# Performance work log

Measured on AMD Instinct MI355X. Metric: run time of the kernel, lower is better.

Reference implementation:

```python
import jax, jax.numpy as jnp
import numpy as np

B, H, W, C = 32, 56, 56, 384
NH, WS, SS = 12, 7, 3
DH = C // NH
N = WS * WS
HID = 4 * C
SCALE = DH ** -0.5


def _make_attn_mask(h, w, ws, ss):
    img = np.zeros((h, w), dtype=np.float32)
    cnt = 0
    for hs in (slice(0, -ws), slice(-ws, -ss), slice(-ss, None)):
        for wsl in (slice(0, -ws), slice(-ws, -ss), slice(-ss, None)):
            img[hs, wsl] = cnt
            cnt += 1
    mw = img.reshape(h // ws, ws, w // ws, ws).transpose(0, 2, 1, 3).reshape(-1, ws * ws)
    diff = mw[:, None, :] - mw[:, :, None]  # (nW, n, n)
    return np.where(diff != 0, np.float32(-100.0), np.float32(0.0))


def _make_rel_pos_index(ws):
    coords = np.stack(np.meshgrid(np.arange(ws), np.arange(ws), indexing='ij')).reshape(2, -1)
    rel = (coords[:, :, None] - coords[:, None, :]).transpose(1, 2, 0)  # (n, n, 2)
    rel[..., 0] += ws - 1
    rel[..., 1] += ws - 1
    rel[..., 0] *= 2 * ws - 1
    return rel.sum(-1)  # (n, n)


ATTN_MASK = jnp.asarray(_make_attn_mask(H, W, WS, SS))          # (nW, n, n)
REL_IDX = jnp.asarray(_make_rel_pos_index(WS))                   # (n, n)


def layernorm(x, g, b, eps):
    mu = jnp.mean(x, axis=-1, keepdims=True)
    var = jnp.var(x, axis=-1, keepdims=True)
    return (x - mu) * jax.lax.rsqrt(var + eps) * g + b


def window_partition(x, ws):
    b, h, w, c = x.shape
    x = x.reshape(b, h // ws, ws, w // ws, ws, c)
    return x.transpose(0, 1, 3, 2, 4, 5).reshape(-1, ws, ws, c)


def window_reverse(windows, ws, h, w):
    b = windows.shape[0] // ((h // ws) * (w // ws))
    x = windows.reshape(b, h // ws, w // ws, ws, ws, -1)
    return x.transpose(0, 1, 3, 2, 4, 5).reshape(b, h, w, -1)


def setup_inputs() -> dict:
    key = jax.random.key(0)
    ks = jax.random.split(key, 8)
    d = {
        'x': jax.random.normal(ks[0], (B, H * W, C), dtype=jnp.float32),
        'ln1_g': jnp.ones((C,), jnp.float32), 'ln1_b': jnp.zeros((C,), jnp.float32),
        'qkv_w': jax.random.normal(ks[1], (C, 3 * C), jnp.float32) * 0.02,
        'qkv_b': jnp.zeros((3 * C,), jnp.float32),
        'proj_w': jax.random.normal(ks[2], (C, C), jnp.float32) * 0.02,
        'proj_b': jnp.zeros((C,), jnp.float32),
        'rpb_table': jax.random.normal(ks[3], ((2 * WS - 1) ** 2, NH), jnp.float32) * 0.02,
        'ln2_g': jnp.ones((C,), jnp.float32), 'ln2_b': jnp.zeros((C,), jnp.float32),
        'ffln_g': jnp.ones((C,), jnp.float32), 'ffln_b': jnp.zeros((C,), jnp.float32),
        'ff1_w': jax.random.normal(ks[4], (C, HID), jnp.float32) * 0.02,
        'ff1_b': jnp.zeros((HID,), jnp.float32),
        'ff2_w': jax.random.normal(ks[5], (HID, C), jnp.float32) * 0.02,
        'ff2_b': jnp.zeros((C,), jnp.float32),
    }
    return d


def reference(x, ln1_g, ln1_b, qkv_w, qkv_b, proj_w, proj_b, rpb_table,
              ln2_g, ln2_b, ffln_g, ffln_b, ff1_w, ff1_b, ff2_w, ff2_b):
    b = x.shape[0]
    shortcut = x
    xn = layernorm(x, ln1_g, ln1_b, 1e-5).reshape(b, H, W, C)
    shifted = jnp.roll(xn, shift=(-SS, -SS), axis=(1, 2))
    xw = window_partition(shifted, WS).reshape(-1, N, C)  # (b*nW, n, c)
    Bw = xw.shape[0]
    nW = Bw // b

    qkv = (xw @ qkv_w + qkv_b).reshape(Bw, N, 3, NH, DH).transpose(2, 0, 3, 1, 4)
    q, k, v = qkv[0], qkv[1], qkv[2]  # (Bw, nh, n, dh)
    dots = jnp.einsum('bhnd,bhmd->bhnm', q, k) * SCALE

    bias = rpb_table[REL_IDX.reshape(-1)].reshape(N, N, NH).transpose(2, 0, 1)  # (nh, n, n)
    attn = dots + bias[None]
    attn = attn.reshape(b, nW, NH, N, N) + ATTN_MASK[None, :, None, :, :]
    attn = jax.nn.softmax(attn.reshape(Bw, NH, N, N), axis=-1)

    out = jnp.einsum('bhnm,bhmd->bhnd', attn, v)
    out = out.transpose(0, 2, 1, 3).reshape(Bw, N, C)
    out = out @ proj_w + proj_b

    out = window_reverse(out.reshape(-1, WS, WS, C), WS, H, W)
    out = jnp.roll(out, shift=(SS, SS), axis=(1, 2)).reshape(b, H * W, C)

    x = shortcut + out
    y = layernorm(x, ln2_g, ln2_b, 1e-5)
    y = layernorm(y, ffln_g, ffln_b, 1e-6)
    y = jax.nn.gelu(y @ ff1_w + ff1_b, approximate=False) @ ff2_w + ff2_b
    return x + y
```

## Files before the change

### kernel.cpp

```cpp
#include <hip/hip_runtime.h>
#include <hip/hip_bf16.h>

typedef short bf16x8 __attribute__((ext_vector_type(8)));
typedef short short4v __attribute__((ext_vector_type(4)));
typedef float f32x4  __attribute__((ext_vector_type(4)));

static constexpr float SCALE = 0.17677669529663687f;

__device__ __forceinline__ void gload_lds16(const void* g, void* l) {
  __builtin_amdgcn_global_load_lds(
      (const __attribute__((address_space(1))) unsigned int*)g,
      (__attribute__((address_space(3))) unsigned int*)l, 16, 0, 0);
}

__device__ __forceinline__ size_t win_to_nat(int t) {
  int win = t / 49; int n = t - win * 49;
  int bb = win >> 6; int wimg = win & 63;
  int hb = wimg >> 3, wb = wimg & 7;
  int nr = n / 7, nc = n - nr * 7;
  int hh = hb * 7 + nr + 3; if (hh >= 56) hh -= 56;
  int ww = wb * 7 + nc + 3; if (ww >= 56) ww -= 56;
  return (size_t)bb * 3136 + (size_t)hh * 56 + ww;
}

__device__ __forceinline__ float gelu_fast(float x) {
  float t = __expf(-1.702f * x);
  return x / (1.f + t);
}

__global__ __launch_bounds__(256)
void k_transpose(const float* __restrict__ W, __hip_bfloat16* __restrict__ Wt,
                 int K, int N) {
  __shared__ float tile[32][33];
  int tx = threadIdx.x & 31, ty = threadIdx.x >> 5;
  int tc = blockIdx.x, tr = blockIdx.y;
#pragma unroll
  for (int r = 0; r < 32; r += 8)
    tile[r + ty][tx] = W[(size_t)(tr * 32 + r + ty) * N + tc * 32 + tx];
  __syncthreads();
#pragma unroll
  for (int r = 0; r < 32; r += 8)
    Wt[(size_t)(tc * 32 + r + ty) * K + tr * 32 + tx] =
        __float2bfloat16(tile[tx][r + ty]);
}

__global__ __launch_bounds__(256)
void k_ln1(const float* __restrict__ x, const float* __restrict__ gw,
           const float* __restrict__ bw, __hip_bfloat16* __restrict__ xw) {
  int lane = threadIdx.x & 63;
  int t = blockIdx.x * 4 + (threadIdx.x >> 6);
  size_t nt = win_to_nat(t);
  const float* xr = x + nt * 384;
  float4 a  = *(const float4*)(xr + lane * 4);
  float2 c2 = *(const float2*)(xr + 256 + lane * 2);
  float v[6] = {a.x, a.y, a.z, a.w, c2.x, c2.y};
  int c0 = lane * 4, c1 = 256 + lane * 2;
  int ch[6] = {c0, c0 + 1, c0 + 2, c0 + 3, c1, c1 + 1};
  float s = 0.f, q = 0.f;
#pragma unroll
  for (int i = 0; i < 6; i++) { s += v[i]; q += v[i] * v[i]; }
#pragma unroll
  for (int m = 1; m < 64; m <<= 1) { s += __shfl_xor(s, m); q += __shfl_xor(q, m); }
  float mean = s * (1.f / 384.f);
  float rstd = rsqrtf(q * (1.f / 384.f) - mean * mean + 1e-5f);
  __hip_bfloat16* o = xw + (size_t)t * 384;
#pragma unroll
  for (int i = 0; i < 6; i++)
    o[ch[i]] = __float2bfloat16((v[i] - mean) * rstd * gw[ch[i]] + bw[ch[i]]);
}

__global__ __launch_bounds__(256)
void k_ln2ff(const float* __restrict__ xres, const float* __restrict__ g2,
             const float* __restrict__ b2, const float* __restrict__ gf,
             const float* __restrict__ bf_, __hip_bfloat16* __restrict__ yln) {
  int lane = threadIdx.x & 63;
  int t = blockIdx.x * 4 + (threadIdx.x >> 6);
  const float* xr = xres + (size_t)t * 384;
  float4 a  = *(const float4*)(xr + lane * 4);
  float2 c2 = *(const float2*)(xr + 256 + lane * 2);
  float v[6] = {a.x, a.y, a.z, a.w, c2.x, c2.y};
  int c0 = lane * 4, c1 = 256 + lane * 2;
  int ch[6] = {c0, c0 + 1, c0 + 2, c0 + 3, c1, c1 + 1};
  float s = 0.f, q = 0.f;
#pragma unroll
  for (int i = 0; i < 6; i++) { s += v[i]; q += v[i] * v[i]; }
#pragma unroll
  for (int m = 1; m < 64; m <<= 1) { s += __shfl_xor(s, m); q += __shfl_xor(q, m); }
  float mean = s * (1.f / 384.f);
  float rstd = rsqrtf(q * (1.f / 384.f) - mean * mean + 1e-5f);
  float y1[6];
  s = 0.f; q = 0.f;
#pragma unroll
  for (int i = 0; i < 6; i++) {
    y1[i] = (v[i] - mean) * rstd * g2[ch[i]] + b2[ch[i]];
    s += y1[i]; q += y1[i] * y1[i];
  }
#pragma unroll
  for (int m = 1; m < 64; m <<= 1) { s += __shfl_xor(s, m); q += __shfl_xor(q, m); }
  float m2 = s * (1.f / 384.f);
  float r2 = rsqrtf(q * (1.f / 384.f) - m2 * m2 + 1e-6f);
  __hip_bfloat16* o = yln + (size_t)t * 384;
#pragma unroll
  for (int i = 0; i < 6; i++)
    o[ch[i]] = __float2bfloat16((y1[i] - m2) * r2 * gf[ch[i]] + bf_[ch[i]]);
}

enum { EPI_QKV = 0, EPI_PROJ = 1, EPI_FF1 = 2, EPI_FF2 = 3 };

template <int EPI>
__global__ __launch_bounds__(256)
void k_gemm(const __hip_bfloat16* __restrict__ A, const __hip_bfloat16* __restrict__ Wt,
            const float* __restrict__ bias, int K, int nCol, int cpx,
            const float* __restrict__ aux,
            float* __restrict__ out_f,
            __hip_bfloat16* __restrict__ out_b) {
  __shared__ __hip_bfloat16 LB[24576];
  int tid = threadIdx.x;
  int lane = tid & 63, w = tid >> 6;
  int g = lane >> 4, r16 = lane & 15;
  int wr = w >> 1, wc = w & 1;

  int bid = blockIdx.x;
  int wg = (bid & 7) * cpx + (bid >> 3);
  int rB = wg / nCol;
  int rowBlk = rB * 128;
  int colBlk = (wg - rB * nCol) * 128;

  int s2 = (tid & 7) ^ ((tid >> 3) & 7);
  int srow = 2 * (tid >> 3) + (s2 >> 2);
  int cch = s2 & 3;
  const __hip_bfloat16* PA = A + (size_t)(rowBlk + srow) * K + cch * 8;
  const __hip_bfloat16* PB = Wt + (size_t)(colBlk + srow) * K + cch * 8;

#define STG(NB, T)                                                            \
  {                                                                           \
    int k0s = (T) << 5;                                                       \
    _Pragma("unroll") for (int j = 0; j < 2; j++) {                           \
      gload_lds16(PA + (size_t)j * 64 * K + k0s, &LB[(NB) * 4096 + j * 2048 + w * 512]); \
      gload_lds16(PB + (size_t)j * 64 * K + k0s, &LB[12288 + (NB) * 4096 + j * 2048 + w * 512]); \
    }                                                                         \
  }

  int rslot = (g + ((r16 & 1) << 2)) ^ (r16 >> 1);
  int aBase = (wr * 32 + (r16 >> 1)) * 64 + rslot * 8;
  int bBase = 12288 + (wc * 32 + (r16 >> 1)) * 64 + rslot * 8;

  f32x4 acc[4][4] = {};
  const int nt = K >> 5;

  STG(0, 0)
  STG(1, 1)

#define STEP(CB, SB, T)                                                       \
  {                                                                           \
    if ((T) + 1 < nt) {                                                       \
      asm volatile("s_waitcnt vmcnt(4)" ::: "memory");                        \
    } else {                                                                  \
      asm volatile("s_waitcnt vmcnt(0)" ::: "memory");                        \
    }                                                                         \
    __builtin_amdgcn_s_barrier();                \
    asm volatile("" ::: "memory");                                            \
    bf16x8 a[4], b[4];                                                        \
    _Pragma("unroll") for (int mi = 0; mi < 4; mi++)                          \
      a[mi] = *(const bf16x8*)(&LB[(CB) * 4096 + aBase + mi * 512]);          \
    _Pragma("unroll") for (int ni = 0; ni < 4; ni++)                          \
      b[ni] = *(const bf16x8*)(&LB[(CB) * 4096 + bBase + ni * 512]);          \
    if ((T) + 2 < nt) STG(SB, (T) + 2)                                        \
    __builtin_amdgcn_s_setprio(1);                                            \
    _Pragma("unroll") for (int mi = 0; mi < 4; mi++)                          \
      _Pragma("unroll") for (int ni = 0; ni < 4; ni++)                        \
        acc[mi][ni] = __builtin_amdgcn_mfma_f32_16x16x32_bf16(                \
            b[ni], a[mi], acc[mi][ni], 0, 0, 0);                              \
    __builtin_amdgcn_s_setprio(0);                                            \
  }

  for (int t = 0; t < nt; t += 3) {
    STEP(0, 2, t)
    STEP(1, 0, t + 1)
    STEP(2, 1, t + 2)
  }
#undef STEP
#undef STG

  if constexpr (EPI == EPI_QKV || EPI == EPI_FF1) {
    __hip_bfloat16* EP = &LB[w * 4096];
#pragma unroll
    for (int ni = 0; ni < 4; ni++) {
      float4 b4 = *(const float4*)(bias + colBlk + wc * 64 + ni * 16 + g * 4);
#pragma unroll
      for (int mi = 0; mi < 4; mi++) {
        float v0 = acc[mi][ni][0] + b4.x, v1 = acc[mi][ni][1] + b4.y,
              v2 = acc[mi][ni][2] + b4.z, v3 = acc[mi][ni][3] + b4.w;
        if constexpr (EPI == EPI_FF1) {
          v0 = gelu_fast(v0); v1 = gelu_fast(v1);
          v2 = gelu_fast(v2); v3 = gelu_fast(v3);
        }
        short4v s4 = {(short)__bfloat16_as_ushort(__float2bfloat16(v0)),
                      (short)__bfloat16_as_ushort(__float2bfloat16(v1)),
                      (short)__bfloat16_as_ushort(__float2bfloat16(v2)),
                      (short)__bfloat16_as_ushort(__float2bfloat16(v3))};
        int row = mi * 16 + r16;
        int ch8 = (ni * 2 + (g >> 1)) ^ (row & 7);
        *(short4v*)(&EP[row * 64 + ch8 * 8 + (g & 1) * 4]) = s4;
      }
    }
#pragma unroll
    for (int j = 0; j < 8; j++) {
      int r = j * 8 + (lane >> 3);
      bf16x8 vv = *(const bf16x8*)(&EP[r * 64 + ((lane & 7) ^ (r & 7)) * 8]);
      int grow = rowBlk + wr * 64 + r;
      int col0 = colBlk + wc * 64 + (lane & 7) * 8;
      if constexpr (EPI == EPI_QKV) {
        int winr = grow / 49, nn = grow - winr * 49;
        int which = col0 / 384; int rem = col0 - which * 384;
        int hh = rem >> 5, dd = rem & 31;
        size_t off = (((size_t)winr * 12 + hh) * 49 + nn) * 32 + dd;
        *(bf16x8*)(out_b + (size_t)which * 38535168u + off) = vv;
      } else {
        *(bf16x8*)(out_b + (size_t)grow * 1536 + col0) = vv;
      }
    }
  } else {
    float* EPF = (float*)LB + w * 2048;
#pragma unroll
    for (int half = 0; half < 2; half++) {
#pragma unroll
      for (int ni = 0; ni < 4; ni++) {
        float4 b4 = *(const float4*)(bias + colBlk + wc * 64 + ni * 16 + g * 4);
#pragma unroll
        for (int mi2 = 0; mi2 < 2; mi2++) {
          int mi = half * 2 + mi2;
          f32x4 v = acc[mi][ni];
          v[0] += b4.x; v[1] += b4.y; v[2] += b4.z; v[3] += b4.w;
          int row = mi2 * 16 + r16;
          int ch4 = (ni * 4 + g) ^ r16;
          *(f32x4*)(&EPF[row * 64 + ch4 * 4]) = v;
        }
      }
#pragma unroll
      for (int j = 0; j < 8; j++) {
        int r = j * 4 + g;
        f32x4 vv = *(const f32x4*)(&EPF[r * 64 + ((r16 ^ (r & 15)) * 4)]);
        int grow = rowBlk + wr * 64 + half * 32 + r;
        int col0 = colBlk + wc * 64 + r16 * 4;
        if constexpr (EPI == EPI_PROJ) {
          size_t nt2 = win_to_nat(grow);
          const float4 a4 = *(const float4*)(aux + nt2 * 384 + col0);
          float4 o4 = {vv[0] + a4.x, vv[1] + a4.y, vv[2] + a4.z, vv[3] + a4.w};
          *(float4*)(out_f + nt2 * 384 + col0) = o4;
        } else {
          const float4 a4 = *(const float4*)(aux + (size_t)grow * 384 + col0);
          float4 o4 = {vv[0] + a4.x, vv[1] + a4.y, vv[2] + a4.z, vv[3] + a4.w};
          *(float4*)(out_f + (size_t)grow * 384 + col0) = o4;
        }
      }
    }
  }
}

__global__ __launch_bounds__(256)
void k_attn(const __hip_bfloat16* __restrict__ q, const __hip_bfloat16* __restrict__ k,
            const __hip_bfloat16* __restrict__ v, const float* __restrict__ rpb,
            __hip_bfloat16* __restrict__ o) {
  __shared__ __hip_bfloat16 P[4][64][72];
  int tid = threadIdx.x;
  int lane = tid & 63, wave = tid >> 6;
  int g = lane >> 4, r16 = lane & 15;
  int gid = blockIdx.x * 4 + wave;
  int wi = gid / 12, h = gid - (gid / 12) * 12;
  int wimg = wi & 63;
  int hb = wimg >> 3, wb = wimg & 7;
  size_t base = ((size_t)wi * 12 + h) * (49 * 32);
  const __hip_bfloat16* qb = q + base;
  const __hip_bfloat16* kb = k + base;
  const __hip_bfloat16* vb = v + base;

  bf16x8 zf = {0, 0, 0, 0, 0, 0, 0, 0};
  bf16x8 qf[4], kf[4];
#pragma unroll
  for (int mi = 0; mi < 4; mi++) {
    int row = mi * 16 + r16;
    qf[mi] = (row < 49) ? *(const bf16x8*)(qb + row * 32 + g * 8) : zf;
    kf[mi] = (row < 49) ? *(const bf16x8*)(kb + row * 32 + g * 8) : zf;
  }
  f32x4 fz = {0.f, 0.f, 0.f, 0.f};
  f32x4 S[4][4];
#pragma unroll
  for (int mi = 0; mi < 4; mi++)
#pragma unroll
    for (int ni = 0; ni < 4; ni++)
      S[mi][ni] = __builtin_amdgcn_mfma_f32_16x16x32_bf16(qf[mi], kf[ni], fz, 0, 0, 0);

  int kiA[4], kjA[4], rkA[4], cvA[4];
#pragma unroll
  for (int ni = 0; ni < 4; ni++) {
    int col = ni * 16 + r16;
    cvA[ni] = (col < 49);
    int ki = col / 7, kj = col - (col / 7) * 7;
    kiA[ni] = ki; kjA[ni] = kj;
    int hg = hb * 7 + ki, wg = wb * 7 + kj;
    int rh = (hg < 49) ? 0 : ((hg < 53) ? 1 : 2);
    int rw = (wg < 49) ? 0 : ((wg < 53) ? 1 : 2);
    rkA[ni] = rh * 3 + rw;
  }

#pragma unroll
  for (int mi = 0; mi < 4; mi++) {
#pragma unroll
    for (int rr = 0; rr < 4; rr++) {
      int row = mi * 16 + g * 4 + rr;
      float sv[4];
      float mx = -1e30f;
      int qi = row / 7, qj = row - (row / 7) * 7;
      int hgq = hb * 7 + qi, wgq = wb * 7 + qj;
      int rhq = (hgq < 49) ? 0 : ((hgq < 53) ? 1 : 2);
      int rwq = (wgq < 49) ? 0 : ((wgq < 53) ? 1 : 2);
      int rq = rhq * 3 + rwq;
#pragma unroll
      for (int ni = 0; ni < 4; ni++) {
        float s = -1e30f;
        if (row < 49 && cvA[ni]) {
          int idx = (qi - kiA[ni] + 6) * 13 + (qj - kjA[ni] + 6);
          float maskv = (rq != rkA[ni]) ? -100.f : 0.f;
          s = S[mi][ni][rr] * SCALE + rpb[idx * 12 + h] + maskv;
        }
        sv[ni] = s;
        mx = fmaxf(mx, s);
      }
#pragma unroll
      for (int m = 1; m <= 8; m <<= 1) mx = fmaxf(mx, __shfl_xor(mx, m));
      float sum = 0.f;
#pragma unroll
      for (int ni = 0; ni < 4; ni++) {
        float p = __expf(sv[ni] - mx);
        sv[ni] = p; sum += p;
      }
#pragma unroll
      for (int m = 1; m <= 8; m <<= 1) sum += __shfl_xor(sum, m);
      float inv = 1.f / sum;
#pragma unroll
      for (int ni = 0; ni < 4; ni++)
        P[wave][row][ni * 16 + r16] = __float2bfloat16(sv[ni] * inv);
    }
  }

  f32x4 O[4][2] = {};
#pragma unroll
  for (int ks = 0; ks < 2; ks++) {
    bf16x8 pf[4];
#pragma unroll
    for (int mi = 0; mi < 4; mi++)
      pf[mi] = *(const bf16x8*)(&P[wave][mi * 16 + r16][ks * 32 + g * 8]);
#pragma unroll
    for (int ni = 0; ni < 2; ni++) {
      bf16x8 vf = zf;
#pragma unroll
      for (int j = 0; j < 8; j++) {
        int m = ks * 32 + g * 8 + j;
        if (m < 49) vf[j] = ((const short*)vb)[m * 32 + ni * 16 + r16];
      }
#pragma unroll
      for (int mi = 0; mi < 4; mi++)
        O[mi][ni] = __builtin_amdgcn_mfma_f32_16x16x32_bf16(pf[mi], vf, O[mi][ni], 0, 0, 0);
    }
  }

#pragma unroll
  for (int mi = 0; mi < 4; mi++)
#pragma unroll
    for (int rr = 0; rr < 4; rr++) {
      int row = mi * 16 + g * 4 + rr;
      if (row < 49) {
#pragma unroll
        for (int ni = 0; ni < 2; ni++) {
          int col = ni * 16 + r16;
          o[(((size_t)wi * 49 + row) * 12 + h) * 32 + col] = __float2bfloat16(O[mi][ni][rr]);
        }
      }
    }
}

extern "C" void kernel_launch(void* const* d_in, const int* in_sizes, int n_in,
                              void* d_out, int out_size, void* d_ws, size_t ws_size,
                              hipStream_t stream) {
  const float* x      = (const float*)d_in[0];
  const float* ln1_g  = (const float*)d_in[1];
  const float* ln1_b  = (const float*)d_in[2];
  const float* qkv_w  = (const float*)d_in[3];
  const float* qkv_b  = (const float*)d_in[4];
  const float* proj_w = (const float*)d_in[5];
  const float* proj_b = (const float*)d_in[6];
  const float* rpb    = (const float*)d_in[7];
  const float* ln2_g  = (const float*)d_in[8];
  const float* ln2_b  = (const float*)d_in[9];
  const float* ffg    = (const float*)d_in[10];
  const float* ffb    = (const float*)d_in[11];
  const float* ff1_w  = (const float*)d_in[12];
  const float* ff1_b  = (const float*)d_in[13];
  const float* ff2_w  = (const float*)d_in[14];
  const float* ff2_b  = (const float*)d_in[15];
  float* out = (float*)d_out;

  char* ws = (char*)d_ws;
  __hip_bfloat16* xw     = (__hip_bfloat16*)ws;
  __hip_bfloat16* qbuf   = (__hip_bfloat16*)(ws + 77070336u);
  __hip_bfloat16* kbuf   = qbuf + 38535168u;
  __hip_bfloat16* vbuf   = kbuf + 38535168u;
  __hip_bfloat16* attn_o = xw;
  __hip_bfloat16* hbuf   = (__hip_bfloat16*)ws;
  float*          x_res  = (float*)(ws + 308281344u);
  __hip_bfloat16* yln    = (__hip_bfloat16*)(ws + 462422016u);
  __hip_bfloat16* qkv_wt = (__hip_bfloat16*)(ws + 539492352u);
  __hip_bfloat16* proj_wt = qkv_wt + 442368u;
  __hip_bfloat16* ff1_wt  = proj_wt + 147456u;
  __hip_bfloat16* ff2_wt  = ff1_wt + 589824u;

  k_transpose<<<dim3(1152 / 32, 384 / 32), dim3(256), 0, stream>>>(qkv_w, qkv_wt, 384, 1152);
  k_transpose<<<dim3(384 / 32, 384 / 32), dim3(256), 0, stream>>>(proj_w, proj_wt, 384, 384);
  k_transpose<<<dim3(1536 / 32, 384 / 32), dim3(256), 0, stream>>>(ff1_w, ff1_wt, 384, 1536);
  k_transpose<<<dim3(384 / 32, 1536 / 32), dim3(256), 0, stream>>>(ff2_w, ff2_wt, 1536, 384);

  k_ln1<<<dim3(25088), dim3(256), 0, stream>>>(x, ln1_g, ln1_b, xw);

  k_gemm<EPI_QKV><<<dim3(7056), dim3(256), 0, stream>>>(xw, qkv_wt, qkv_b, 384, 9, 7056 / 8,
                                                        nullptr, nullptr, qbuf);
  k_attn<<<dim3(6144), dim3(256), 0, stream>>>(qbuf, kbuf, vbuf, rpb, attn_o);
  k_gemm<EPI_PROJ><<<dim3(2352), dim3(256), 0, stream>>>(attn_o, proj_wt, proj_b, 384, 3, 2352 / 8,
                                                         x, x_res, nullptr);
  k_ln2ff<<<dim3(25088), dim3(256), 0, stream>>>(x_res, ln2_g, ln2_b, ffg, ffb, yln);
  k_gemm<EPI_FF1><<<dim3(9408), dim3(256), 0, stream>>>(yln, ff1_wt, ff1_b, 384, 12, 9408 / 8,
                                                        nullptr, nullptr, hbuf);
  k_gemm<EPI_FF2><<<dim3(2352), dim3(256), 0, stream>>>(hbuf, ff2_wt, ff2_b, 1536, 3, 2352 / 8,
                                                        x_res, out, nullptr);
}
```

Measured before the change: 907.3 us.

## Shrink GEMM workgroups to single-wave 64x64 tiles without barriers

```diff
diff --git a/kernel.cpp b/kernel.cpp
--- a/kernel.cpp
+++ b/kernel.cpp
@@ -108,42 +108,39 @@
 enum { EPI_QKV = 0, EPI_PROJ = 1, EPI_FF1 = 2, EPI_FF2 = 3 };
 
 template <int EPI>
-__global__ __launch_bounds__(256)
+__global__ __launch_bounds__(64)
 void k_gemm(const __hip_bfloat16* __restrict__ A, const __hip_bfloat16* __restrict__ Wt,
             const float* __restrict__ bias, int K, int nCol, int cpx,
             const float* __restrict__ aux,
             float* __restrict__ out_f,
             __hip_bfloat16* __restrict__ out_b) {
-  __shared__ __hip_bfloat16 LB[24576];
-  int tid = threadIdx.x;
-  int lane = tid & 63, w = tid >> 6;
+  __shared__ __hip_bfloat16 LB[12288];
+  int lane = threadIdx.x;
   int g = lane >> 4, r16 = lane & 15;
-  int wr = w >> 1, wc = w & 1;
 
   int bid = blockIdx.x;
   int wg = (bid & 7) * cpx + (bid >> 3);
   int rB = wg / nCol;
-  int rowBlk = rB * 128;
-  int colBlk = (wg - rB * nCol) * 128;
-
-  int s2 = (tid & 7) ^ ((tid >> 3) & 7);
-  int srow = 2 * (tid >> 3) + (s2 >> 2);
+  int rowBlk = rB * 64;
+  int colBlk = (wg - rB * nCol) * 64;
+
+  int s2 = (lane & 7) ^ ((lane >> 3) & 7);
+  int srow0 = 2 * (lane >> 3) + (s2 >> 2);
   int cch = s2 & 3;
-  const __hip_bfloat16* PA = A + (size_t)(rowBlk + srow) * K + cch * 8;
-  const __hip_bfloat16* PB = Wt + (size_t)(colBlk + srow) * K + cch * 8;
+  const __hip_bfloat16* PA = A + (size_t)(rowBlk + srow0) * K + cch * 8;
+  const __hip_bfloat16* PB = Wt + (size_t)(colBlk + srow0) * K + cch * 8;
 
 #define STG(NB, T)                                                            \
   {                                                                           \
     int k0s = (T) << 5;                                                       \
-    _Pragma("unroll") for (int j = 0; j < 2; j++) {                           \
-      gload_lds16(PA + (size_t)j * 64 * K + k0s, &LB[(NB) * 4096 + j * 2048 + w * 512]); \
-      gload_lds16(PB + (size_t)j * 64 * K + k0s, &LB[12288 + (NB) * 4096 + j * 2048 + w * 512]); \
+    _Pragma("unroll") for (int p = 0; p < 4; p++) {                           \
+      gload_lds16(PA + (size_t)p * 16 * K + k0s, &LB[(NB) * 4096 + p * 512]); \
+      gload_lds16(PB + (size_t)p * 16 * K + k0s, &LB[(NB) * 4096 + 2048 + p * 512]); \
     }                                                                         \
   }
 
   int rslot = (g + ((r16 & 1) << 2)) ^ (r16 >> 1);
-  int aBase = (wr * 32 + (r16 >> 1)) * 64 + rslot * 8;
-  int bBase = 12288 + (wc * 32 + (r16 >> 1)) * 64 + rslot * 8;
+  int aOff = (r16 >> 1) * 64 + rslot * 8;
 
   f32x4 acc[4][4] = {};
   const int nt = K >> 5;
@@ -154,17 +151,15 @@
 #define STEP(CB, SB, T)                                                       \
   {                                                                           \
     if ((T) + 1 < nt) {                                                       \
-      asm volatile("s_waitcnt vmcnt(4)" ::: "memory");                        \
+      asm volatile("s_waitcnt vmcnt(8)" ::: "memory");     \
     } else {                                                                  \
       asm volatile("s_waitcnt vmcnt(0)" ::: "memory");                        \
     }                                                                         \
-    __builtin_amdgcn_s_barrier();                \
-    asm volatile("" ::: "memory");                                            \
     bf16x8 a[4], b[4];                                                        \
     _Pragma("unroll") for (int mi = 0; mi < 4; mi++)                          \
-      a[mi] = *(const bf16x8*)(&LB[(CB) * 4096 + aBase + mi * 512]);          \
+      a[mi] = *(const bf16x8*)(&LB[(CB) * 4096 + aOff + mi * 512]);           \
     _Pragma("unroll") for (int ni = 0; ni < 4; ni++)                          \
-      b[ni] = *(const bf16x8*)(&LB[(CB) * 4096 + bBase + ni * 512]);          \
+      b[ni] = *(const bf16x8*)(&LB[(CB) * 4096 + 2048 + aOff + ni * 512]);    \
     if ((T) + 2 < nt) STG(SB, (T) + 2)                                        \
     __builtin_amdgcn_s_setprio(1);                                            \
     _Pragma("unroll") for (int mi = 0; mi < 4; mi++)                          \
@@ -183,10 +178,10 @@
 #undef STG
 
   if constexpr (EPI == EPI_QKV || EPI == EPI_FF1) {
-    __hip_bfloat16* EP = &LB[w * 4096];
+    __hip_bfloat16* EP = LB;
 #pragma unroll
     for (int ni = 0; ni < 4; ni++) {
-      float4 b4 = *(const float4*)(bias + colBlk + wc * 64 + ni * 16 + g * 4);
+      float4 b4 = *(const float4*)(bias + colBlk + ni * 16 + g * 4);
 #pragma unroll
       for (int mi = 0; mi < 4; mi++) {
         float v0 = acc[mi][ni][0] + b4.x, v1 = acc[mi][ni][1] + b4.y,
@@ -208,8 +203,8 @@
     for (int j = 0; j < 8; j++) {
       int r = j * 8 + (lane >> 3);
       bf16x8 vv = *(const bf16x8*)(&EP[r * 64 + ((lane & 7) ^ (r & 7)) * 8]);
-      int grow = rowBlk + wr * 64 + r;
-      int col0 = colBlk + wc * 64 + (lane & 7) * 8;
+      int grow = rowBlk + r;
+      int col0 = colBlk + (lane & 7) * 8;
       if constexpr (EPI == EPI_QKV) {
         int winr = grow / 49, nn = grow - winr * 49;
         int which = col0 / 384; int rem = col0 - which * 384;
@@ -221,12 +216,12 @@
       }
     }
   } else {
-    float* EPF = (float*)LB + w * 2048;
+    float* EPF = (float*)LB;
 #pragma unroll
     for (int half = 0; half < 2; half++) {
 #pragma unroll
       for (int ni = 0; ni < 4; ni++) {
-        float4 b4 = *(const float4*)(bias + colBlk + wc * 64 + ni * 16 + g * 4);
+        float4 b4 = *(const float4*)(bias + colBlk + ni * 16 + g * 4);
 #pragma unroll
         for (int mi2 = 0; mi2 < 2; mi2++) {
           int mi = half * 2 + mi2;
@@ -241,8 +236,8 @@
       for (int j = 0; j < 8; j++) {
         int r = j * 4 + g;
         f32x4 vv = *(const f32x4*)(&EPF[r * 64 + ((r16 ^ (r & 15)) * 4)]);
-        int grow = rowBlk + wr * 64 + half * 32 + r;
-        int col0 = colBlk + wc * 64 + r16 * 4;
+        int grow = rowBlk + half * 32 + r;
+        int col0 = colBlk + r16 * 4;
         if constexpr (EPI == EPI_PROJ) {
           size_t nt2 = win_to_nat(grow);
           const float4 a4 = *(const float4*)(aux + nt2 * 384 + col0);
@@ -422,14 +417,14 @@
 
   k_ln1<<<dim3(25088), dim3(256), 0, stream>>>(x, ln1_g, ln1_b, xw);
 
-  k_gemm<EPI_QKV><<<dim3(7056), dim3(256), 0, stream>>>(xw, qkv_wt, qkv_b, 384, 9, 7056 / 8,
+  k_gemm<EPI_QKV><<<dim3(28224), dim3(64), 0, stream>>>(xw, qkv_wt, qkv_b, 384, 18, 28224 / 8,
                                                         nullptr, nullptr, qbuf);
   k_attn<<<dim3(6144), dim3(256), 0, stream>>>(qbuf, kbuf, vbuf, rpb, attn_o);
-  k_gemm<EPI_PROJ><<<dim3(2352), dim3(256), 0, stream>>>(attn_o, proj_wt, proj_b, 384, 3, 2352 / 8,
-                                                         x, x_res, nullptr);
+  k_gemm<EPI_PROJ><<<dim3(9408), dim3(64), 0, stream>>>(attn_o, proj_wt, proj_b, 384, 6, 9408 / 8,
+                                                        x, x_res, nullptr);
   k_ln2ff<<<dim3(25088), dim3(256), 0, stream>>>(x_res, ln2_g, ln2_b, ffg, ffb, yln);
-  k_gemm<EPI_FF1><<<dim3(9408), dim3(256), 0, stream>>>(yln, ff1_wt, ff1_b, 384, 12, 9408 / 8,
+  k_gemm<EPI_FF1><<<dim3(37632), dim3(64), 0, stream>>>(yln, ff1_wt, ff1_b, 384, 24, 37632 / 8,
                                                         nullptr, nullptr, hbuf);
-  k_gemm<EPI_FF2><<<dim3(2352), dim3(256), 0, stream>>>(hbuf, ff2_wt, ff2_b, 1536, 3, 2352 / 8,
-                                                        x_res, out, nullptr);
-}
+  k_gemm<EPI_FF2><<<dim3(9408), dim3(64), 0, stream>>>(hbuf, ff2_wt, ff2_b, 1536, 6, 9408 / 8,
+                                                       x_res, out, nullptr);
+}
```

Result: slower. 1.218 ms (+34.3%).

## Enlarge GEMM tiles to 512x128 with 8 waves and balanced XCD mapping

Applied to the files above, without the earlier changes.

```diff
diff --git a/kernel.cpp b/kernel.cpp
--- a/kernel.cpp
+++ b/kernel.cpp
@@ -108,22 +108,24 @@
 enum { EPI_QKV = 0, EPI_PROJ = 1, EPI_FF1 = 2, EPI_FF2 = 3 };
 
 template <int EPI>
-__global__ __launch_bounds__(256)
+__global__ __launch_bounds__(512, 1)
 void k_gemm(const __hip_bfloat16* __restrict__ A, const __hip_bfloat16* __restrict__ Wt,
-            const float* __restrict__ bias, int K, int nCol, int cpx,
+            const float* __restrict__ bias, int K, int nCol, int nwg,
             const float* __restrict__ aux,
             float* __restrict__ out_f,
             __hip_bfloat16* __restrict__ out_b) {
-  __shared__ __hip_bfloat16 LB[24576];
+  __shared__ __hip_bfloat16 LB[61440];
   int tid = threadIdx.x;
   int lane = tid & 63, w = tid >> 6;
   int g = lane >> 4, r16 = lane & 15;
   int wr = w >> 1, wc = w & 1;
 
   int bid = blockIdx.x;
-  int wg = (bid & 7) * cpx + (bid >> 3);
+  int qch = nwg >> 3, rch = nwg & 7;
+  int xcd = bid & 7, idx = bid >> 3;
+  int wg = (xcd < rch ? xcd * (qch + 1) : rch * (qch + 1) + (xcd - rch) * qch) + idx;
   int rB = wg / nCol;
-  int rowBlk = rB * 128;
+  int rowBlk = rB * 512;
   int colBlk = (wg - rB * nCol) * 128;
 
   int s2 = (tid & 7) ^ ((tid >> 3) & 7);
@@ -135,17 +137,17 @@
 #define STG(NB, T)                                                            \
   {                                                                           \
     int k0s = (T) << 5;                                                       \
-    _Pragma("unroll") for (int j = 0; j < 2; j++) {                           \
-      gload_lds16(PA + (size_t)j * 64 * K + k0s, &LB[(NB) * 4096 + j * 2048 + w * 512]); \
-      gload_lds16(PB + (size_t)j * 64 * K + k0s, &LB[12288 + (NB) * 4096 + j * 2048 + w * 512]); \
-    }                                                                         \
+    _Pragma("unroll") for (int p = 0; p < 4; p++)                             \
+      gload_lds16(PA + (size_t)p * 128 * K + k0s,                             \
+                  &LB[(NB) * 20480 + p * 4096 + w * 512]);                    \
+    gload_lds16(PB + k0s, &LB[(NB) * 20480 + 16384 + w * 512]);               \
   }
 
   int rslot = (g + ((r16 & 1) << 2)) ^ (r16 >> 1);
-  int aBase = (wr * 32 + (r16 >> 1)) * 64 + rslot * 8;
-  int bBase = 12288 + (wc * 32 + (r16 >> 1)) * 64 + rslot * 8;
-
-  f32x4 acc[4][4] = {};
+  int aBase = wr * 4096 + (r16 >> 1) * 64 + rslot * 8;
+  int bBase = 16384 + wc * 2048 + (r16 >> 1) * 64 + rslot * 8;
+
+  f32x4 acc[8][4] = {};
   const int nt = K >> 5;
 
   STG(0, 0)
@@ -154,20 +156,20 @@
 #define STEP(CB, SB, T)                                                       \
   {                                                                           \
     if ((T) + 1 < nt) {                                                       \
-      asm volatile("s_waitcnt vmcnt(4)" ::: "memory");                        \
+      asm volatile("s_waitcnt vmcnt(5)" ::: "memory");                        \
     } else {                                                                  \
       asm volatile("s_waitcnt vmcnt(0)" ::: "memory");                        \
     }                                                                         \
     __builtin_amdgcn_s_barrier();                \
     asm volatile("" ::: "memory");                                            \
-    bf16x8 a[4], b[4];                                                        \
-    _Pragma("unroll") for (int mi = 0; mi < 4; mi++)                          \
-      a[mi] = *(const bf16x8*)(&LB[(CB) * 4096 + aBase + mi * 512]);          \
+    bf16x8 a[8], b[4];                                                        \
+    _Pragma("unroll") for (int mi = 0; mi < 8; mi++)                          \
+      a[mi] = *(const bf16x8*)(&LB[(CB) * 20480 + aBase + mi * 512]);         \
     _Pragma("unroll") for (int ni = 0; ni < 4; ni++)                          \
-      b[ni] = *(const bf16x8*)(&LB[(CB) * 4096 + bBase + ni * 512]);          \
+      b[ni] = *(const bf16x8*)(&LB[(CB) * 20480 + bBase + ni * 512]);         \
     if ((T) + 2 < nt) STG(SB, (T) + 2)                                        \
     __builtin_amdgcn_s_setprio(1);                                            \
-    _Pragma("unroll") for (int mi = 0; mi < 4; mi++)                          \
+    _Pragma("unroll") for (int mi = 0; mi < 8; mi++)                          \
       _Pragma("unroll") for (int ni = 0; ni < 4; ni++)                        \
         acc[mi][ni] = __builtin_amdgcn_mfma_f32_16x16x32_bf16(                \
             b[ni], a[mi], acc[mi][ni], 0, 0, 0);                              \
@@ -185,51 +187,55 @@
   if constexpr (EPI == EPI_QKV || EPI == EPI_FF1) {
     __hip_bfloat16* EP = &LB[w * 4096];
 #pragma unroll
-    for (int ni = 0; ni < 4; ni++) {
-      float4 b4 = *(const float4*)(bias + colBlk + wc * 64 + ni * 16 + g * 4);
-#pragma unroll
-      for (int mi = 0; mi < 4; mi++) {
-        float v0 = acc[mi][ni][0] + b4.x, v1 = acc[mi][ni][1] + b4.y,
-              v2 = acc[mi][ni][2] + b4.z, v3 = acc[mi][ni][3] + b4.w;
-        if constexpr (EPI == EPI_FF1) {
-          v0 = gelu_fast(v0); v1 = gelu_fast(v1);
-          v2 = gelu_fast(v2); v3 = gelu_fast(v3);
-        }
-        short4v s4 = {(short)__bfloat16_as_ushort(__float2bfloat16(v0)),
-                      (short)__bfloat16_as_ushort(__float2bfloat16(v1)),
-                      (short)__bfloat16_as_ushort(__float2bfloat16(v2)),
-                      (short)__bfloat16_as_ushort(__float2bfloat16(v3))};
-        int row = mi * 16 + r16;
-        int ch8 = (ni * 2 + (g >> 1)) ^ (row & 7);
-        *(short4v*)(&EP[row * 64 + ch8 * 8 + (g & 1) * 4]) = s4;
-      }
-    }
-#pragma unroll
-    for (int j = 0; j < 8; j++) {
-      int r = j * 8 + (lane >> 3);
-      bf16x8 vv = *(const bf16x8*)(&EP[r * 64 + ((lane & 7) ^ (r & 7)) * 8]);
-      int grow = rowBlk + wr * 64 + r;
-      int col0 = colBlk + wc * 64 + (lane & 7) * 8;
-      if constexpr (EPI == EPI_QKV) {
-        int winr = grow / 49, nn = grow - winr * 49;
-        int which = col0 / 384; int rem = col0 - which * 384;
-        int hh = rem >> 5, dd = rem & 31;
-        size_t off = (((size_t)winr * 12 + hh) * 49 + nn) * 32 + dd;
-        *(bf16x8*)(out_b + (size_t)which * 38535168u + off) = vv;
-      } else {
-        *(bf16x8*)(out_b + (size_t)grow * 1536 + col0) = vv;
+    for (int h = 0; h < 2; h++) {
+#pragma unroll
+      for (int ni = 0; ni < 4; ni++) {
+        float4 b4 = *(const float4*)(bias + colBlk + wc * 64 + ni * 16 + g * 4);
+#pragma unroll
+        for (int mi2 = 0; mi2 < 4; mi2++) {
+          int mi = h * 4 + mi2;
+          float v0 = acc[mi][ni][0] + b4.x, v1 = acc[mi][ni][1] + b4.y,
+                v2 = acc[mi][ni][2] + b4.z, v3 = acc[mi][ni][3] + b4.w;
+          if constexpr (EPI == EPI_FF1) {
+            v0 = gelu_fast(v0); v1 = gelu_fast(v1);
+            v2 = gelu_fast(v2); v3 = gelu_fast(v3);
+          }
+          short4v s4 = {(short)__bfloat16_as_ushort(__float2bfloat16(v0)),
+                        (short)__bfloat16_as_ushort(__float2bfloat16(v1)),
+                        (short)__bfloat16_as_ushort(__float2bfloat16(v2)),
+                        (short)__bfloat16_as_ushort(__float2bfloat16(v3))};
+          int row = mi2 * 16 + r16;
+          int ch8 = (ni * 2 + (g >> 1)) ^ (row & 7);
+          *(short4v*)(&EP[row * 64 + ch8 * 8 + (g & 1) * 4]) = s4;
+        }
+      }
+#pragma unroll
+      for (int j = 0; j < 8; j++) {
+        int r = j * 8 + (lane >> 3);
+        bf16x8 vv = *(const bf16x8*)(&EP[r * 64 + ((lane & 7) ^ (r & 7)) * 8]);
+        int grow = rowBlk + wr * 128 + h * 64 + r;
+        int col0 = colBlk + wc * 64 + (lane & 7) * 8;
+        if constexpr (EPI == EPI_QKV) {
+          int winr = grow / 49, nn = grow - winr * 49;
+          int which = col0 / 384; int rem = col0 - which * 384;
+          int hh = rem >> 5, dd = rem & 31;
+          size_t off = (((size_t)winr * 12 + hh) * 49 + nn) * 32 + dd;
+          *(bf16x8*)(out_b + (size_t)which * 38535168u + off) = vv;
+        } else {
+          *(bf16x8*)(out_b + (size_t)grow * 1536 + col0) = vv;
+        }
       }
     }
   } else {
     float* EPF = (float*)LB + w * 2048;
 #pragma unroll
-    for (int half = 0; half < 2; half++) {
+    for (int q2 = 0; q2 < 4; q2++) {
 #pragma unroll
       for (int ni = 0; ni < 4; ni++) {
         float4 b4 = *(const float4*)(bias + colBlk + wc * 64 + ni * 16 + g * 4);
 #pragma unroll
         for (int mi2 = 0; mi2 < 2; mi2++) {
-          int mi = half * 2 + mi2;
+          int mi = q2 * 2 + mi2;
           f32x4 v = acc[mi][ni];
           v[0] += b4.x; v[1] += b4.y; v[2] += b4.z; v[3] += b4.w;
           int row = mi2 * 16 + r16;
@@ -241,7 +247,7 @@
       for (int j = 0; j < 8; j++) {
         int r = j * 4 + g;
         f32x4 vv = *(const f32x4*)(&EPF[r * 64 + ((r16 ^ (r & 15)) * 4)]);
-        int grow = rowBlk + wr * 64 + half * 32 + r;
+        int grow = rowBlk + wr * 128 + q2 * 32 + r;
         int col0 = colBlk + wc * 64 + r16 * 4;
         if constexpr (EPI == EPI_PROJ) {
           size_t nt2 = win_to_nat(grow);
@@ -422,14 +428,14 @@
 
   k_ln1<<<dim3(25088), dim3(256), 0, stream>>>(x, ln1_g, ln1_b, xw);
 
-  k_gemm<EPI_QKV><<<dim3(7056), dim3(256), 0, stream>>>(xw, qkv_wt, qkv_b, 384, 9, 7056 / 8,
+  k_gemm<EPI_QKV><<<dim3(1764), dim3(512), 0, stream>>>(xw, qkv_wt, qkv_b, 384, 9, 1764,
                                                         nullptr, nullptr, qbuf);
   k_attn<<<dim3(6144), dim3(256), 0, stream>>>(qbuf, kbuf, vbuf, rpb, attn_o);
-  k_gemm<EPI_PROJ><<<dim3(2352), dim3(256), 0, stream>>>(attn_o, proj_wt, proj_b, 384, 3, 2352 / 8,
-                                                         x, x_res, nullptr);
+  k_gemm<EPI_PROJ><<<dim3(588), dim3(512), 0, stream>>>(attn_o, proj_wt, proj_b, 384, 3, 588,
+                                                        x, x_res, nullptr);
   k_ln2ff<<<dim3(25088), dim3(256), 0, stream>>>(x_res, ln2_g, ln2_b, ffg, ffb, yln);
-  k_gemm<EPI_FF1><<<dim3(9408), dim3(256), 0, stream>>>(yln, ff1_wt, ff1_b, 384, 12, 9408 / 8,
+  k_gemm<EPI_FF1><<<dim3(2352), dim3(512), 0, stream>>>(yln, ff1_wt, ff1_b, 384, 12, 2352,
                                                         nullptr, nullptr, hbuf);
-  k_gemm<EPI_FF2><<<dim3(2352), dim3(256), 0, stream>>>(hbuf, ff2_wt, ff2_b, 1536, 3, 2352 / 8,
-                                                        x_res, out, nullptr);
-}
+  k_gemm<EPI_FF2><<<dim3(588), dim3(512), 0, stream>>>(hbuf, ff2_wt, ff2_b, 1536, 3, 588,
+                                                       x_res, out, nullptr);
+}
```

Measured after the change: 961.1 us. 1.06x slower.
